# Kernel tuning notes

Measured on AMD Instinct MI355X. Metric: run time of the kernel, lower is better.

The kernel has to match this reference:

```python
import jax, jax.numpy as jnp
import numpy as np

GAMMA = 1.0
BANDWIDTH = 0.0  # 0 disables the Sakoe-Chiba band, matching `0 < bandwidth` checks
INF = 1e30       # finite sentinel standing in for np.inf (keeps grads NaN-free)


def setup_inputs() -> dict:
    key = jax.random.key(0)
    D = jax.random.uniform(key, (64, 512, 512), dtype=jnp.float32)
    return {"D": D}


def _softdtw_forward(D):
    """Anti-diagonal wavefront soft-DTW DP. Returns R[:, N, M] (shape (B,))."""
    B, N, M = D.shape
    T = N + M - 1  # diagonals d = i + j, d in [2, N+M]; step t <-> d = t + 2

    # Rearrange D along anti-diagonals: Ddiag[t, b, i-1] = D[b, i-1, (t+2-i)-1]
    i_idx = jnp.arange(1, N + 1)                       # (N,) DP row index i
    t_idx = jnp.arange(T)                              # (T,)
    j_idx = t_idx[:, None] + 2 - i_idx[None, :]        # (T, N) DP col index j
    valid = (j_idx >= 1) & (j_idx <= M)
    if BANDWIDTH > 0:
        valid = valid & (jnp.abs(i_idx[None, :] - j_idx) <= BANDWIDTH)
    jc = jnp.clip(j_idx - 1, 0, M - 1)                 # (T, N) safe gather col
    Ddiag = D[:, jnp.broadcast_to(i_idx[None, :] - 1, (T, N)), jc]  # (B, T, N)
    Ddiag = jnp.transpose(Ddiag, (1, 0, 2))            # (T, B, N)

    # Carry: two previous anti-diagonals of R, indexed by i = 0..N.
    # prev2 = diag d-2 (init d=0: R[0,0]=0), prev1 = diag d-1 (init d=1: all inf).
    prev2 = jnp.full((B, N + 1), INF, D.dtype).at[:, 0].set(0.0)
    prev1 = jnp.full((B, N + 1), INF, D.dtype)

    def step(carry, inputs):
        p2, p1 = carry
        Dd, vmask = inputs                             # (B, N), (N,)
        # neighbors for cells i = 1..N on current diag:
        #   R[i-1, j-1] -> p2[i-1], R[i-1, j] -> p1[i-1], R[i, j-1] -> p1[i]
        r = jnp.stack([p2[:, :-1], p1[:, :-1], p1[:, 1:]]) * (-1.0 / GAMMA)  # (3,B,N)
        rmax = jnp.max(r, axis=0)
        softmin = -GAMMA * (jnp.log(jnp.sum(jnp.exp(r - rmax), axis=0)) + rmax)
        new = jnp.where(vmask[None, :], Dd + softmin, INF)
        new_full = jnp.concatenate(
            [jnp.full((B, 1), INF, new.dtype), new], axis=1)  # i = 0 border
        return (p1, new_full), None

    (_, last), _ = jax.lax.scan(step, (prev2, prev1), (Ddiag, valid))
    return last[:, N]  # R[:, N, M] == R[:, -2, -2]


def reference(D):
    return _softdtw_forward(D)
```

## Files before the change

### kernel.cpp

```cpp
#include <hip/hip_runtime.h>
#include <stdint.h>
#include <math.h>


namespace {
constexpr int NWAVE = 4;
constexpr int DELTA = 96;
constexpr int MCOLS = 512;
constexpr int LOCAL = MCOLS + 63;
constexpr int NCHUNK = 54;
constexpr int BROW = 608;
constexpr int RW = 65;
constexpr float LN2 = 0.69314718055994530942f;
constexpr float L2E = 1.44269504088896340736f;
}

using f4 = __attribute__((ext_vector_type(4))) float;
using u32x4 = __attribute__((ext_vector_type(4))) unsigned int;

__device__ __forceinline__ float dpp_shr1(float v) {
  return __int_as_float(__builtin_amdgcn_update_dpp(0, __float_as_int(v), 0x138, 0xf, 0xf, true));
}
__device__ __forceinline__ int dpp_shr1_i(int v) {
  return __builtin_amdgcn_update_dpp(0, v, 0x138, 0xf, 0xf, true);
}
__device__ __forceinline__ float rdlane(float v, int lane) {
  return __int_as_float(__builtin_amdgcn_readlane(__float_as_int(v), lane));
}
__device__ __forceinline__ void packw(const f4& g, uint32_t* p) {
  uint32_t w0, w1;
  asm("v_cvt_pk_bf16_f32 %0, %1, %2" : "=v"(w0) : "v"(g[0]), "v"(g[1]));
  asm("v_cvt_pk_bf16_f32 %0, %1, %2" : "=v"(w1) : "v"(g[2]), "v"(g[3]));
  p[0] = w0;
  p[1] = w1;
}

struct Pref {
  uint32_t W[9];
  uint32_t V[9];
  float bv;
  int Eb;
  int Ead;
};

__device__ __forceinline__ void prefetch(Pref& P, int tn, int w, int l,
                                         const uint32_t* __restrict__ q1,
                                         const uint32_t* __restrict__ q2,
                                         const float* __restrict__ brd,
                                         const int* __restrict__ brdE) {
  if (tn < 0 || tn >= LOCAL) return;
  const int e0 = ((tn - l) & 127) >> 1;
#pragma unroll
  for (int k = 0; k < 9; ++k) {
    P.W[k] = q1[(e0 + k) & 63];
    P.V[k] = q2[(e0 + k) & 63];
  }
  if (w > 0 && tn < 512) {
    const int j = l & 15;
    P.bv = brd[tn + j];
    P.Eb = brdE[(tn >> 4) + (j ? 4 : 3)];
    P.Ead = brdE[3];
  }
}

template <bool G>
__device__ __forceinline__ void steps16(const Pref& P, int t0, int l, int tid,
                                        bool isL0, bool par, uint32_t shE,
                                        uint32_t shO, float rsc, float curv,
                                        float* __restrict__ bwr,
                                        float& x1, float& x2, float& areg) {
#pragma unroll
  for (int s = 0; s < 16; ++s) {
    const int c = t0 + s - l;
    uint32_t wd, vd;
    if ((s & 1) == 0) {
      wd = P.W[s >> 1];
      vd = P.V[s >> 1];
    } else {
      wd = par ? P.W[(s + 1) >> 1] : P.W[s >> 1];
      vd = par ? P.V[(s + 1) >> 1] : P.V[s >> 1];
    }
    const uint32_t sh = (s & 1) ? shO : shE;
    const float d1 = __uint_as_float((wd << sh) & 0xffff0000u);
    const float d2 = __uint_as_float((vd << sh) & 0xffff0000u);
    const float k1 = __builtin_amdgcn_exp2f(d1 * -L2E);
    const float k2 = __builtin_amdgcn_exp2f(d2 * -L2E);
    float aa = areg;
    if (G) aa = (tid == 0 && c == 0) ? 1.0f : aa;
    const float k1s1 = k1 * (aa + x1);
    const float k2s2 = k2 * (x1 + x2);
    const float bsh = dpp_shr1(x2) * rsc;
    const float bb = isL0 ? rdlane(curv, s) : bsh;
    const float x1n = fmaf(k1, bb, k1s1);
    const float x2n = fmaf(k2, x1n, k2s2);
    if (G) {
      const bool act = (unsigned)c < 512u;
      const int idx = act ? c : (int)(544u + ((unsigned)c & 63u));
      bwr[idx] = x2n;
      x1 = act ? x1n : x1;
      x2 = act ? x2n : x2;
    } else {
      bwr[c] = x2n;
      x1 = x1n;
      x2 = x2n;
    }
    areg = bb;
  }
}

#define STAGE_ISSUE(CS) do {                                                        \
    const int v0_ = voBase + ((CS) << 2);                                           \
    asm volatile("buffer_load_dwordx4 %0, %1, %2, 0 offen" : "=v"(g0) : "v"(v0_), "s"(srd));             \
    asm volatile("buffer_load_dwordx4 %0, %1, %2, 0 offen" : "=v"(g1) : "v"(v0_ + 1*32768), "s"(srd));   \
    asm volatile("buffer_load_dwordx4 %0, %1, %2, 0 offen" : "=v"(g2) : "v"(v0_ + 2*32768), "s"(srd));   \
    asm volatile("buffer_load_dwordx4 %0, %1, %2, 0 offen" : "=v"(g3) : "v"(v0_ + 3*32768), "s"(srd));   \
    asm volatile("buffer_load_dwordx4 %0, %1, %2, 0 offen" : "=v"(g4) : "v"(v0_ + 4*32768), "s"(srd));   \
    asm volatile("buffer_load_dwordx4 %0, %1, %2, 0 offen" : "=v"(g5) : "v"(v0_ + 5*32768), "s"(srd));   \
    asm volatile("buffer_load_dwordx4 %0, %1, %2, 0 offen" : "=v"(g6) : "v"(v0_ + 6*32768), "s"(srd));   \
    asm volatile("buffer_load_dwordx4 %0, %1, %2, 0 offen" : "=v"(g7) : "v"(v0_ + 7*32768), "s"(srd));   \
} while (0)

#define STAGE_WRITE(CS) do {                                                        \
    asm volatile("s_waitcnt vmcnt(0)"                                               \
        : "+v"(g0), "+v"(g1), "+v"(g2), "+v"(g3),                                   \
          "+v"(g4), "+v"(g5), "+v"(g6), "+v"(g7)::);                                \
    const int ew_ = ((((CS) & 127) >> 1) + ((l & 3) << 1));                         \
    uint32_t* rp_ = &dring[w][l >> 2][ew_];                                         \
    packw(g0, rp_);            packw(g1, rp_ + 16 * RW);                            \
    packw(g2, rp_ + 32 * RW);  packw(g3, rp_ + 48 * RW);                            \
    packw(g4, rp_ + 64 * RW);  packw(g5, rp_ + 80 * RW);                            \
    packw(g6, rp_ + 96 * RW);  packw(g7, rp_ + 112 * RW);                           \
} while (0)

#define BODY(PC, PN, MC) do {                                                       \
    const int t0_ = 16 * (MC) - ow;                                                 \
    const bool doStage_ = (t0_ >= 0) && (t0_ <= 480);     \
    if (doStage_) STAGE_ISSUE(t0_ + 16);                                            \
    if (t0_ >= 0 && t0_ < LOCAL) {                                                  \
      const int ENpre_ = dpp_shr1_i(E);                                             \
      const bool inact_ = (x1 == 0.0f) && (x2 == 0.0f);                             \
      if (w > 0 && t0_ == 0) E = PC.Ead;             \
      else if (inact_ && !isL0) E = ENpre_;                \
      float curv_ = 0.0f;                                                           \
      if (w > 0 && t0_ < 512) {                                                     \
        const int E0_ = __builtin_amdgcn_readfirstlane(E);                          \
        curv_ = ldexpf(PC.bv, PC.Eb - E0_);              \
      }                                                                             \
      if (l == 63) bwrE[t0_ >> 4] = E;              \
      const int EN2_ = dpp_shr1_i(E);                                               \
      int dE_ = EN2_ - E;                                                           \
      dE_ = dE_ < -126 ? -126 : (dE_ > 126 ? 126 : dE_);                            \
      const float rsc_ = __int_as_float((127 + dE_) << 23);                         \
      if (t0_ >= 64 && t0_ <= 496)                                                  \
        steps16<false>(PC, t0_, l, tid, isL0, par, shE, shO, rsc_, curv_, bwr,      \
                       x1, x2, areg);                                               \
      else                                                                          \
        steps16<true>(PC, t0_, l, tid, isL0, par, shE, shO, rsc_, curv_, bwr,       \
                      x1, x2, areg);                                                \
                        \
      const int bx_ = (__float_as_int(x1) >> 23) & 255;                             \
      const int by_ = (__float_as_int(x2) >> 23) & 255;                             \
      int exm_ = bx_ > by_ ? bx_ : by_;                                             \
      int sh_ = (exm_ > 0) ? (117 - exm_) : 0;                                      \
      sh_ = sh_ < -110 ? -110 : sh_;                                                \
      const float sc_ = __int_as_float((127 + sh_) << 23);                          \
      x1 *= sc_; x2 *= sc_; areg *= sc_; E -= sh_;                                  \
    }                                                                               \
    if (doStage_) STAGE_WRITE(t0_ + 16);            \
         \
         \
    prefetch(PN, t0_ + 16, w, l, q1p, q2p, brd, brdE);                              \
         \
         \
    asm volatile("s_waitcnt lgkmcnt(0)\n\ts_barrier" ::: "memory");                 \
} while (0)

__global__ __launch_bounds__(256, 1) void sdtw_kernel(const float* __restrict__ D,
                                                      float* __restrict__ out) {
  static_assert(NCHUNK % 2 == 0, "loop is 2x unrolled");
  __shared__ uint32_t dring[NWAVE][128][RW];
  __shared__ float bnd[NWAVE + 1][BROW];
  __shared__ int bndE[NWAVE][36];
  const int tid = threadIdx.x;
  const int w = tid >> 6, l = tid & 63, b = blockIdx.x;

  u32x4 srd;
  const uint64_t base = (uint64_t)(const void*)D;
  srd[0] = (unsigned)base;
  srd[1] = (unsigned)(base >> 32) & 0xffffu;
  srd[2] = 64u * 512u * 512u * 4u;
  srd[3] = 0x00020000u;

  const int ow = w * DELTA;
  const bool isL0 = (l == 0);
  const bool par = (l & 1) != 0;
  const uint32_t shE = par ? 0u : 16u;
  const uint32_t shO = par ? 16u : 0u;
  const int voBase = (((b << 9) + (w << 7) + (l >> 2)) << 11) + ((l & 3) << 4);

  float* __restrict__ bwr = &bnd[(w == NWAVE - 1) ? NWAVE : w][0];
  float* __restrict__ brd = &bnd[(w == 0) ? 0 : (w - 1)][0];
  int* __restrict__ bwrE = &bndE[w][0];
  int* __restrict__ brdE = &bndE[(w == 0) ? 0 : (w - 1)][0];
  const uint32_t* __restrict__ q1p = &dring[w][2 * l][0];
  const uint32_t* __restrict__ q2p = &dring[w][2 * l + 1][0];

  float x1 = 0.0f, x2 = 0.0f, areg = 0.0f;
  int E = 0;

  f4 g0, g1, g2, g3, g4, g5, g6, g7;
  Pref PA{}, PB{};

  STAGE_ISSUE(0);
  STAGE_WRITE(0);
  prefetch(PA, -ow, w, l, q1p, q2p, brd, brdE);

  for (int mc = 0; mc < NCHUNK; mc += 2) {
    BODY(PA, PB, mc);
    BODY(PB, PA, mc + 1);
  }

  if (tid == NWAVE * 64 - 1) {
    const float Rv = -(__builtin_amdgcn_logf(x2) + (float)E);
    out[b] = Rv * LN2;
  }
}

extern "C" void kernel_launch(void* const* d_in, const int* in_sizes, int n_in,
                              void* d_out, int out_size, void* d_ws, size_t ws_size,
                              hipStream_t stream) {
  const float* D = (const float*)d_in[0];
  float* out = (float*)d_out;
  hipLaunchKernelGGL(sdtw_kernel, dim3(64), dim3(NWAVE * 64), 0, stream, D, out);
}
```

Baseline: 98.34 us.

## Batch boundary writes to LDS and use asm ds_read2 prefetch with partial waitcnt

Result: faster. 91.77 us (-6.7%).

```diff
diff --git a/kernel.cpp b/kernel.cpp
--- a/kernel.cpp
+++ b/kernel.cpp
@@ -9,14 +9,15 @@
 constexpr int MCOLS = 512;
 constexpr int LOCAL = MCOLS + 63;
 constexpr int NCHUNK = 54;
-constexpr int BROW = 608;
-constexpr int RW = 65;
+constexpr int BROW = 528;
+constexpr int RW = 66;
 constexpr float LN2 = 0.69314718055994530942f;
 constexpr float L2E = 1.44269504088896340736f;
 }
 
 using f4 = __attribute__((ext_vector_type(4))) float;
 using u32x4 = __attribute__((ext_vector_type(4))) unsigned int;
+using u2v = __attribute__((ext_vector_type(2))) unsigned int;
 
 __device__ __forceinline__ float dpp_shr1(float v) {
   return __int_as_float(__builtin_amdgcn_update_dpp(0, __float_as_int(v), 0x138, 0xf, 0xf, true));
@@ -27,12 +28,11 @@
 __device__ __forceinline__ float rdlane(float v, int lane) {
   return __int_as_float(__builtin_amdgcn_readlane(__float_as_int(v), lane));
 }
-__device__ __forceinline__ void packw(const f4& g, uint32_t* p) {
-  uint32_t w0, w1;
-  asm("v_cvt_pk_bf16_f32 %0, %1, %2" : "=v"(w0) : "v"(g[0]), "v"(g[1]));
-  asm("v_cvt_pk_bf16_f32 %0, %1, %2" : "=v"(w1) : "v"(g[2]), "v"(g[3]));
-  p[0] = w0;
-  p[1] = w1;
+__device__ __forceinline__ uint2 packw2(const f4& g) {
+  uint32_t a, b;
+  asm("v_cvt_pk_bf16_f32 %0, %1, %2" : "=v"(a) : "v"(g[0]), "v"(g[1]));
+  asm("v_cvt_pk_bf16_f32 %0, %1, %2" : "=v"(b) : "v"(g[2]), "v"(g[3]));
+  return make_uint2(a, b);
 }
 
 struct Pref {
@@ -43,40 +43,48 @@
   int Ead;
 };
 
-__device__ __forceinline__ void prefetch(Pref& P, int tn, int w, int l,
-                                         const uint32_t* __restrict__ q1,
-                                         const uint32_t* __restrict__ q2,
-                                         const float* __restrict__ brd,
-                                         const int* __restrict__ brdE) {
-  if (tn < 0 || tn >= LOCAL) return;
-  const int e0 = ((tn - l) & 127) >> 1;
-#pragma unroll
-  for (int k = 0; k < 9; ++k) {
-    P.W[k] = q1[(e0 + k) & 63];
-    P.V[k] = q2[(e0 + k) & 63];
-  }
-  if (w > 0 && tn < 512) {
-    const int j = l & 15;
-    P.bv = brd[tn + j];
-    P.Eb = brdE[(tn >> 4) + (j ? 4 : 3)];
-    P.Ead = brdE[3];
-  }
+__device__ __forceinline__ void prefetch_asm(Pref& P, int tn, int w, int l,
+                                             uint32_t ringB, uint32_t brdB,
+                                             uint32_t brdEB) {
+  int tnc = tn < 0 ? 0 : (tn > LOCAL - 1 ? LOCAL - 1 : tn);
+  const int e0 = ((tnc - l) & 127) >> 1;
+  u2v p0, p1, p2, p3, p4, p5, p6, p7, p8;
+  uint32_t a0 = ringB + (((e0 + 0) & 63) << 2);
+  asm volatile("ds_read2_b32 %0, %1 offset0:0 offset1:66" : "=v"(p0) : "v"(a0) : "memory");
+#define RD2(P_, K_) { uint32_t a_ = ringB + (((e0 + (K_)) & 63) << 2);              \
+    asm volatile("ds_read2_b32 %0, %1 offset0:0 offset1:66" : "=v"(P_) : "v"(a_)); }
+  RD2(p1, 1) RD2(p2, 2) RD2(p3, 3) RD2(p4, 4) RD2(p5, 5) RD2(p6, 6) RD2(p7, 7) RD2(p8, 8)
+#undef RD2
+  const int j = l & 15;
+  int bi = tnc + j; bi = bi > 511 ? 511 : bi;
+  uint32_t bvu, ebu, eau;
+  { uint32_t a_ = brdB + (bi << 2);
+    asm volatile("ds_read_b32 %0, %1" : "=v"(bvu) : "v"(a_)); }
+  int ei = (tnc >> 4) + (j ? 4 : 3); ei = ei > 35 ? 35 : ei;
+  { uint32_t a_ = brdEB + (ei << 2);
+    asm volatile("ds_read_b32 %0, %1" : "=v"(ebu) : "v"(a_)); }
+  asm volatile("ds_read_b32 %0, %1" : "=v"(eau) : "v"(brdEB + 12));
+  P.W[0] = p0[0]; P.V[0] = p0[1]; P.W[1] = p1[0]; P.V[1] = p1[1];
+  P.W[2] = p2[0]; P.V[2] = p2[1]; P.W[3] = p3[0]; P.V[3] = p3[1];
+  P.W[4] = p4[0]; P.V[4] = p4[1]; P.W[5] = p5[0]; P.V[5] = p5[1];
+  P.W[6] = p6[0]; P.V[6] = p6[1]; P.W[7] = p7[0]; P.V[7] = p7[1];
+  P.W[8] = p8[0]; P.V[8] = p8[1];
+  P.bv = __uint_as_float(bvu); P.Eb = (int)ebu; P.Ead = (int)eau;
 }
 
 template <bool G>
 __device__ __forceinline__ void steps16(const Pref& P, int t0, int l, int tid,
                                         bool isL0, bool par, uint32_t shE,
                                         uint32_t shO, float rsc, float curv,
-                                        float* __restrict__ bwr,
-                                        float& x1, float& x2, float& areg) {
+                                        f4& vb0, f4& vb1, f4& vb2, f4& vb3,
+                                        float& cF, float& x1, float& x2,
+                                        float& areg) {
+  vb0[0] = cF;
 #pragma unroll
   for (int s = 0; s < 16; ++s) {
-    const int c = t0 + s - l;
     uint32_t wd, vd;
-    if ((s & 1) == 0) {
-      wd = P.W[s >> 1];
-      vd = P.V[s >> 1];
-    } else {
+    if ((s & 1) == 0) { wd = P.W[s >> 1]; vd = P.V[s >> 1]; }
+    else {
       wd = par ? P.W[(s + 1) >> 1] : P.W[s >> 1];
       vd = par ? P.V[(s + 1) >> 1] : P.V[s >> 1];
     }
@@ -86,21 +94,27 @@
     const float k1 = __builtin_amdgcn_exp2f(d1 * -L2E);
     const float k2 = __builtin_amdgcn_exp2f(d2 * -L2E);
     float aa = areg;
-    if (G) aa = (tid == 0 && c == 0) ? 1.0f : aa;
+    int c = 0;
+    if (G) {
+      c = t0 + s - l;
+      aa = (tid == 0 && c == 0) ? 1.0f : aa;
+    }
     const float k1s1 = k1 * (aa + x1);
     const float k2s2 = k2 * (x1 + x2);
     const float bsh = dpp_shr1(x2) * rsc;
     const float bb = isL0 ? rdlane(curv, s) : bsh;
     const float x1n = fmaf(k1, bb, k1s1);
     const float x2n = fmaf(k2, x1n, k2s2);
+    if (s < 3)       vb0[s + 1] = x2n;
+    else if (s < 7)  vb1[s - 3] = x2n;
+    else if (s < 11) vb2[s - 7] = x2n;
+    else if (s < 15) vb3[s - 11] = x2n;
+    else             cF = x2n;
     if (G) {
       const bool act = (unsigned)c < 512u;
-      const int idx = act ? c : (int)(544u + ((unsigned)c & 63u));
-      bwr[idx] = x2n;
       x1 = act ? x1n : x1;
       x2 = act ? x2n : x2;
     } else {
-      bwr[c] = x2n;
       x1 = x1n;
       x2 = x2n;
     }
@@ -124,17 +138,24 @@
     asm volatile("s_waitcnt vmcnt(0)"                                               \
         : "+v"(g0), "+v"(g1), "+v"(g2), "+v"(g3),                                   \
           "+v"(g4), "+v"(g5), "+v"(g6), "+v"(g7)::);                                \
-    const int ew_ = ((((CS) & 127) >> 1) + ((l & 3) << 1));                         \
-    uint32_t* rp_ = &dring[w][l >> 2][ew_];                                         \
-    packw(g0, rp_);            packw(g1, rp_ + 16 * RW);                            \
-    packw(g2, rp_ + 32 * RW);  packw(g3, rp_ + 48 * RW);                            \
-    packw(g4, rp_ + 64 * RW);  packw(g5, rp_ + 80 * RW);                            \
-    packw(g6, rp_ + 96 * RW);  packw(g7, rp_ + 112 * RW);                           \
+    const int ew_ = (((CS) & 127) >> 1) + ((l & 3) << 1);                           \
+    const int r_ = l >> 2;                                                          \
+    *(uint2*)&dring[w][r_][ew_]       = packw2(g0);                                 \
+    *(uint2*)&dring[w][r_ + 16][ew_]  = packw2(g1);                                 \
+    *(uint2*)&dring[w][r_ + 32][ew_]  = packw2(g2);                                 \
+    *(uint2*)&dring[w][r_ + 48][ew_]  = packw2(g3);                                 \
+    *(uint2*)&dring[w][r_ + 64][ew_]  = packw2(g4);                                 \
+    *(uint2*)&dring[w][r_ + 80][ew_]  = packw2(g5);                                 \
+    *(uint2*)&dring[w][r_ + 96][ew_]  = packw2(g6);                                 \
+    *(uint2*)&dring[w][r_ + 112][ew_] = packw2(g7);                                 \
 } while (0)
 
 #define BODY(PC, PN, MC) do {                                                       \
     const int t0_ = 16 * (MC) - ow;                                                 \
-    const bool doStage_ = (t0_ >= 0) && (t0_ <= 480);     \
+             \
+    asm volatile("s_waitcnt lgkmcnt(0)" ::: "memory");                              \
+    __builtin_amdgcn_sched_barrier(0);                                              \
+    const bool doStage_ = (t0_ >= 0) && (t0_ <= 480);                               \
     if (doStage_) STAGE_ISSUE(t0_ + 16);                                            \
     if (t0_ >= 0 && t0_ < LOCAL) {                                                  \
       const int ENpre_ = dpp_shr1_i(E);                                             \
@@ -146,17 +167,17 @@
         const int E0_ = __builtin_amdgcn_readfirstlane(E);                          \
         curv_ = ldexpf(PC.bv, PC.Eb - E0_);              \
       }                                                                             \
-      if (l == 63) bwrE[t0_ >> 4] = E;              \
+      if (l == 63) bwrE[t0_ >> 4] = E;                                              \
       const int EN2_ = dpp_shr1_i(E);                                               \
       int dE_ = EN2_ - E;                                                           \
       dE_ = dE_ < -126 ? -126 : (dE_ > 126 ? 126 : dE_);                            \
       const float rsc_ = __int_as_float((127 + dE_) << 23);                         \
       if (t0_ >= 64 && t0_ <= 496)                                                  \
-        steps16<false>(PC, t0_, l, tid, isL0, par, shE, shO, rsc_, curv_, bwr,      \
-                       x1, x2, areg);                                               \
+        steps16<false>(PC, t0_, l, tid, isL0, par, shE, shO, rsc_, curv_,           \
+                       vb0, vb1, vb2, vb3, cF, x1, x2, areg);                       \
       else                                                                          \
-        steps16<true>(PC, t0_, l, tid, isL0, par, shE, shO, rsc_, curv_, bwr,       \
-                      x1, x2, areg);                                                \
+        steps16<true>(PC, t0_, l, tid, isL0, par, shE, shO, rsc_, curv_,            \
+                      vb0, vb1, vb2, vb3, cF, x1, x2, areg);                        \
                         \
       const int bx_ = (__float_as_int(x1) >> 23) & 255;                             \
       const int by_ = (__float_as_int(x2) >> 23) & 255;                             \
@@ -165,21 +186,25 @@
       sh_ = sh_ < -110 ? -110 : sh_;                                                \
       const float sc_ = __int_as_float((127 + sh_) << 23);                          \
       x1 *= sc_; x2 *= sc_; areg *= sc_; E -= sh_;                                  \
+              \
+      if (t0_ >= 64 && t0_ <= 560 && l == 63) {                                     \
+        f4* bp_ = (f4*)&bwr[t0_ - 64];                                              \
+        bp_[0] = vb0; bp_[1] = vb1; bp_[2] = vb2; bp_[3] = vb3;                     \
+      }                                                                             \
     }                                                                               \
-    if (doStage_) STAGE_WRITE(t0_ + 16);            \
-         \
-         \
-    prefetch(PN, t0_ + 16, w, l, q1p, q2p, brd, brdE);                              \
-         \
-         \
-    asm volatile("s_waitcnt lgkmcnt(0)\n\ts_barrier" ::: "memory");                 \
+    if (doStage_) STAGE_WRITE(t0_ + 16);                                            \
+    prefetch_asm(PN, 16 * ((MC) + 1) - ow, w, l, ringB, brdB, brdEB);               \
+          \
+          \
+    asm volatile("s_waitcnt lgkmcnt(12)" ::: "memory");                             \
+    __builtin_amdgcn_s_barrier();                                                   \
 } while (0)
 
 __global__ __launch_bounds__(256, 1) void sdtw_kernel(const float* __restrict__ D,
                                                       float* __restrict__ out) {
   static_assert(NCHUNK % 2 == 0, "loop is 2x unrolled");
   __shared__ uint32_t dring[NWAVE][128][RW];
-  __shared__ float bnd[NWAVE + 1][BROW];
+  __shared__ alignas(16) float bnd[NWAVE + 1][BROW];
   __shared__ int bndE[NWAVE][36];
   const int tid = threadIdx.x;
   const int w = tid >> 6, l = tid & 63, b = blockIdx.x;
@@ -199,21 +224,22 @@
   const int voBase = (((b << 9) + (w << 7) + (l >> 2)) << 11) + ((l & 3) << 4);
 
   float* __restrict__ bwr = &bnd[(w == NWAVE - 1) ? NWAVE : w][0];
-  float* __restrict__ brd = &bnd[(w == 0) ? 0 : (w - 1)][0];
   int* __restrict__ bwrE = &bndE[w][0];
-  int* __restrict__ brdE = &bndE[(w == 0) ? 0 : (w - 1)][0];
-  const uint32_t* __restrict__ q1p = &dring[w][2 * l][0];
-  const uint32_t* __restrict__ q2p = &dring[w][2 * l + 1][0];
+  const uint32_t ringB = (uint32_t)(uintptr_t)&dring[w][2 * l][0];
+  const uint32_t brdB = (uint32_t)(uintptr_t)&bnd[(w == 0) ? 0 : (w - 1)][0];
+  const uint32_t brdEB = (uint32_t)(uintptr_t)&bndE[(w == 0) ? 0 : (w - 1)][0];
 
   float x1 = 0.0f, x2 = 0.0f, areg = 0.0f;
   int E = 0;
 
   f4 g0, g1, g2, g3, g4, g5, g6, g7;
+  f4 vb0{}, vb1{}, vb2{}, vb3{};
+  float cF = 0.0f;
   Pref PA{}, PB{};
 
   STAGE_ISSUE(0);
   STAGE_WRITE(0);
-  prefetch(PA, -ow, w, l, q1p, q2p, brd, brdE);
+  prefetch_asm(PA, -ow, w, l, ringB, brdB, brdEB);
 
   for (int mc = 0; mc < NCHUNK; mc += 2) {
     BODY(PA, PB, mc);
```
